# Optimization experiments

Measured on AMD Instinct MI355X. Metric: run time of the kernel, lower is better.

Reference implementation:

```python
import jax, jax.numpy as jnp
import numpy as np

NUM_EXPERTS = 64
TOP_K = 8
ALPHA = 0.001


def setup_inputs() -> dict:
    key = jax.random.key(0)
    k1, k2 = jax.random.split(key)
    hidden_states = jax.random.normal(k1, (16384, 2048), dtype=jnp.float32)
    # nn.Linear(D, E) weight has shape (E, D); init ~ N(0, 1/sqrt(D))
    weight = jax.random.normal(k2, (NUM_EXPERTS, 2048), dtype=jnp.float32) / jnp.sqrt(2048.0)
    return {"hidden_states": hidden_states, "weight": weight}


def reference(hidden_states, weight):
    # Router logits: (N, E)
    logits = jnp.einsum("nd,ed->ne", hidden_states, weight)
    scores = jax.nn.softmax(logits, axis=-1)

    # top-k (lax.top_k returns sorted values; torch used sorted=False, same set)
    topk_weights, topk_indices = jax.lax.top_k(scores, TOP_K)  # (N, K)
    topk_weights = topk_weights / jnp.sum(topk_weights, axis=-1, keepdims=True)

    # Aux load-balancing loss (training path). Instead of materializing a
    # (N, K, E) one-hot tensor, count tokens per expert with a scatter-add.
    num_tokens = hidden_states.shape[0]
    counts = jnp.zeros((NUM_EXPERTS,), dtype=jnp.float32).at[topk_indices.ravel()].add(1.0)
    tokens_per_expert = counts / (num_tokens * TOP_K)
    mean_prob = jnp.mean(scores, axis=0)  # (E,)
    aux_loss = ALPHA * NUM_EXPERTS * jnp.sum(tokens_per_expert * mean_prob)

    return topk_weights, topk_indices, aux_loss
```

## Files before the change

kernel.cpp:

```cpp
#include <hip/hip_runtime.h>
#include <hip/hip_bf16.h>

#define N_TOKENS 16384
#define DIM      2048
#define NEXP     64
#define TOPK     8
#define LOSCALE  2048.0f
#define NBLOCKS  512
#define TOKPB    32
#define LSTRIDE  66
#define NREP     32
#define NROUNDS  16
#define NBUF     3
#define BUFSZ    (TOKPB * 128)

typedef _Float16 half8   __attribute__((ext_vector_type(8)));
typedef float    floatx4 __attribute__((ext_vector_type(4)));

__global__ __launch_bounds__(256) void wprep_kernel(const float* __restrict__ W,
                                                    _Float16* __restrict__ Whi,
                                                    _Float16* __restrict__ Wlo) {
    int i = blockIdx.x * 256 + threadIdx.x;
    float w = W[i];
    _Float16 h = (_Float16)w;
    Whi[i] = h;
    Wlo[i] = (_Float16)((w - (float)h) * LOSCALE);
}

__device__ __forceinline__ void gl_lds16(const float* src, float* lds_base, int byteoff) {
    __builtin_amdgcn_global_load_lds(
        (const __attribute__((address_space(1))) unsigned int*)src,
        (__attribute__((address_space(3))) unsigned int*)((char*)lds_base + byteoff),
        16, 0, 0);
}

__device__ __forceinline__ void split8(const floatx4& f0, const floatx4& f1,
                                       half8& H, half8& L) {
    #pragma unroll
    for (int j = 0; j < 4; ++j) {
        _Float16 h = (_Float16)f0[j];
        H[j] = h; L[j] = (_Float16)((f0[j] - (float)h) * LOSCALE);
    }
    #pragma unroll
    for (int j = 0; j < 4; ++j) {
        _Float16 h = (_Float16)f1[j];
        H[4 + j] = h; L[4 + j] = (_Float16)((f1[j] - (float)h) * LOSCALE);
    }
}

__global__ __launch_bounds__(256) void moe_kernel(const float* __restrict__ A,
                                                  const _Float16* __restrict__ Whi,
                                                  const _Float16* __restrict__ Wlo,
                                                  float* __restrict__ out_w,
                                                  float* __restrict__ out_i,
                                                  float* __restrict__ out_aux,
                                                  float* __restrict__ cnt_ws,
                                                  float* __restrict__ sp_ws,
                                                  unsigned int* __restrict__ ticket) {
    __shared__ float stage[NBUF][BUFSZ];
    __shared__ float xch[TOKPB * LSTRIDE];
    __shared__ float s_cnt[NEXP];
    __shared__ float s_sp[NEXP];
    __shared__ int   s_last;

    const int tid   = threadIdx.x;
    const int lane  = tid & 63;
    const int wv    = tid >> 6;
    const int row16 = lane & 15;
    const int quad  = lane >> 4;
    const int tbase = blockIdx.x * TOKPB;

    if (tid < NEXP) { s_cnt[tid] = 0.f; s_sp[tid] = 0.f; }

    const float* asrc[4];
    #pragma unroll
    for (int j = 0; j < 4; ++j) {
        int tok  = (wv * 4 + j) * 2 + (lane >> 5);
        int colb = ((lane & 31) * 16) ^ ((tok & 7) << 4);
        asrc[j] = (const float*)((const char*)(A + (size_t)(tbase + tok) * DIM) + colb);
    }

    const _Float16* bhp = Whi + (size_t)(wv * 16 + row16) * DIM + quad * 8;
    const _Float16* blp = Wlo + (size_t)(wv * 16 + row16) * DIM + quad * 8;

    floatx4 acc0[2] = {};
    floatx4 acc1[2] = {};

    const int c0 = (quad * 8) ^ ((row16 & 7) * 4);

    #pragma unroll
    for (int j = 0; j < 4; ++j) gl_lds16(asrc[j],       &stage[0][0], (wv * 4 + j) * 1024);
    #pragma unroll
    for (int j = 0; j < 4; ++j) gl_lds16(asrc[j] + 128, &stage[1][0], (wv * 4 + j) * 1024);

    half8 bh[4], bl[4];
    #pragma unroll
    for (int c = 0; c < 4; ++c) {
        bh[c] = *(const half8*)(bhp + c * 32);
        bl[c] = *(const half8*)(blp + c * 32);
    }
    asm volatile("s_waitcnt vmcnt(12)" ::: "memory");
    __builtin_amdgcn_sched_barrier(0);
    __builtin_amdgcn_s_barrier();
    __builtin_amdgcn_sched_barrier(0);

    #pragma unroll
    for (int r = 0; r < NROUNDS; ++r) {
        const float* rb = &stage[r % 3][0];

        if (r < NROUNDS - 2) {
            #pragma unroll
            for (int j = 0; j < 4; ++j)
                gl_lds16(asrc[j] + (r + 2) * 128, &stage[(r + 2) % 3][0], (wv * 4 + j) * 1024);
        }

        #pragma unroll
        for (int I = 0; I < 4; ++I) {
            const float* p0 = rb + row16 * 128 + I * 32;
            floatx4 f0 = *(const floatx4*)(p0 + c0);
            floatx4 f1 = *(const floatx4*)(p0 + (c0 ^ 4));
            half8 ah, al; split8(f0, f1, ah, al);
            acc0[0] = __builtin_amdgcn_mfma_f32_16x16x32_f16(ah, bh[I], acc0[0], 0, 0, 0);
            acc1[0] = __builtin_amdgcn_mfma_f32_16x16x32_f16(ah, bl[I], acc1[0], 0, 0, 0);
            acc1[0] = __builtin_amdgcn_mfma_f32_16x16x32_f16(al, bh[I], acc1[0], 0, 0, 0);

            const float* p1 = rb + (16 + row16) * 128 + I * 32;
            f0 = *(const floatx4*)(p1 + c0);
            f1 = *(const floatx4*)(p1 + (c0 ^ 4));
            split8(f0, f1, ah, al);
            acc0[1] = __builtin_amdgcn_mfma_f32_16x16x32_f16(ah, bh[I], acc0[1], 0, 0, 0);
            acc1[1] = __builtin_amdgcn_mfma_f32_16x16x32_f16(ah, bl[I], acc1[1], 0, 0, 0);
            acc1[1] = __builtin_amdgcn_mfma_f32_16x16x32_f16(al, bh[I], acc1[1], 0, 0, 0);

            if (r < NROUNDS - 1) {
                bh[I] = *(const half8*)(bhp + ((r + 1) * 4 + I) * 32);
                bl[I] = *(const half8*)(blp + ((r + 1) * 4 + I) * 32);
            }
        }

        if (r < NROUNDS - 2) {
            asm volatile("s_waitcnt vmcnt(12)" ::: "memory");
        } else if (r == NROUNDS - 2) {
            asm volatile("s_waitcnt vmcnt(8)" ::: "memory");
        }
        if (r < NROUNDS - 1) {
            __builtin_amdgcn_sched_barrier(0);
            __builtin_amdgcn_s_barrier();
            __builtin_amdgcn_sched_barrier(0);
        }
    }

    const float inv = 1.0f / LOSCALE;
    #pragma unroll
    for (int mt = 0; mt < 2; ++mt)
        #pragma unroll
        for (int reg = 0; reg < 4; ++reg) {
            int tok = mt * 16 + quad * 4 + reg;
            xch[tok * LSTRIDE + wv * 16 + row16] = acc0[mt][reg] + acc1[mt][reg] * inv;
        }
    __syncthreads();

    float sp = 0.f, cnt = 0.f;
    for (int i = 0; i < 8; ++i) {
        int t = wv * 8 + i;
        float lg = xch[t * LSTRIDE + lane];

        float m = lg;
        #pragma unroll
        for (int off = 32; off; off >>= 1) m = fmaxf(m, __shfl_xor(m, off));
        float e = expf(lg - m);
        float ssum = e;
        #pragma unroll
        for (int off = 32; off; off >>= 1) ssum += __shfl_xor(ssum, off);
        float score = e / ssum;
        sp += score;

        int rank = 0;
        #pragma unroll
        for (int j = 0; j < 64; ++j) {
            float sj = __shfl(score, j);
            rank += (sj > score) || (sj == score && j < lane);
        }
        bool sel = rank < TOPK;

        float v = sel ? score : 0.f;
        #pragma unroll
        for (int off = 32; off; off >>= 1) v += __shfl_xor(v, off);

        if (sel) {
            out_w[(size_t)(tbase + t) * TOPK + rank] = score / v;
            out_i[(size_t)(tbase + t) * TOPK + rank] = (float)lane;
            cnt += 1.f;
        }
    }

    atomicAdd(&s_sp[lane], sp);
    atomicAdd(&s_cnt[lane], cnt);
    __syncthreads();
    const int rep = (blockIdx.x & (NREP - 1)) * NEXP;
    if (tid < 64)       atomicAdd(&cnt_ws[rep + tid], s_cnt[tid]);
    else if (tid < 128) atomicAdd(&sp_ws[rep + tid - 64], s_sp[tid - 64]);

    __threadfence();
    __syncthreads();
    if (tid == 0)
        s_last = (atomicAdd(ticket, 1u) == (unsigned)(gridDim.x - 1));
    __syncthreads();
    if (s_last && tid < 64) {
        float c = 0.f, p = 0.f;
        #pragma unroll
        for (int rr = 0; rr < NREP; ++rr) {
            c += atomicAdd(&cnt_ws[rr * NEXP + tid], 0.f);
            p += atomicAdd(&sp_ws [rr * NEXP + tid], 0.f);
        }
        float v = (c / (float)(N_TOKENS * TOPK)) * (p / (float)N_TOKENS);
        #pragma unroll
        for (int off = 32; off; off >>= 1) v += __shfl_xor(v, off);
        if (tid == 0) out_aux[0] = 0.001f * (float)NEXP * v;
    }
}

extern "C" void kernel_launch(void* const* d_in, const int* in_sizes, int n_in,
                              void* d_out, int out_size, void* d_ws, size_t ws_size,
                              hipStream_t stream) {
    const float* A = (const float*)d_in[0];
    const float* W = (const float*)d_in[1];
    float* out = (float*)d_out;

    _Float16*     whi    = (_Float16*)d_ws;
    _Float16*     wlo    = whi + (size_t)NEXP * DIM;
    float*        cnt_ws = (float*)(wlo + (size_t)NEXP * DIM);
    float*        sp_ws  = cnt_ws + (size_t)NREP * NEXP;
    unsigned int* ticket = (unsigned int*)(sp_ws + (size_t)NREP * NEXP);

    hipMemsetAsync(cnt_ws, 0, 2 * NREP * NEXP * sizeof(float) + sizeof(unsigned int), stream);

    hipLaunchKernelGGL(wprep_kernel, dim3(NEXP * DIM / 256), dim3(256), 0, stream,
                       W, whi, wlo);

    float* out_w = out;
    float* out_i = out + (size_t)N_TOKENS * TOPK;
    float* out_a = out + 2 * (size_t)N_TOKENS * TOPK;

    hipLaunchKernelGGL(moe_kernel, dim3(NBLOCKS), dim3(256), 0, stream,
                       A, whi, wlo, out_w, out_i, out_a, cnt_ws, sp_ws, ticket);
}
```

Before: 256.6 us.

## Restructure A staging into double-buffered 256-wide K rounds with padded LDS rows

Measured after the change: 253.0 us. About the same (-1.4%).

```diff
diff --git a/kernel.cpp b/kernel.cpp
--- a/kernel.cpp
+++ b/kernel.cpp
@@ -10,9 +10,9 @@
 #define TOKPB    32
 #define LSTRIDE  66
 #define NREP     32
-#define NROUNDS  16
-#define NBUF     3
-#define BUFSZ    (TOKPB * 128)
+#define KROUND   256
+#define NR       8
+#define SPAD     260
 
 typedef _Float16 half8   __attribute__((ext_vector_type(8)));
 typedef float    floatx4 __attribute__((ext_vector_type(4)));
@@ -27,10 +27,10 @@
     Wlo[i] = (_Float16)((w - (float)h) * LOSCALE);
 }
 
-__device__ __forceinline__ void gl_lds16(const float* src, float* lds_base, int byteoff) {
+__device__ __forceinline__ void gl_lds16(const float* src, float* lds_dst) {
     __builtin_amdgcn_global_load_lds(
         (const __attribute__((address_space(1))) unsigned int*)src,
-        (__attribute__((address_space(3))) unsigned int*)((char*)lds_base + byteoff),
+        (__attribute__((address_space(3))) unsigned int*)lds_dst,
         16, 0, 0);
 }
 
@@ -57,7 +57,7 @@
                                                   float* __restrict__ cnt_ws,
                                                   float* __restrict__ sp_ws,
                                                   unsigned int* __restrict__ ticket) {
-    __shared__ float stage[NBUF][BUFSZ];
+    __shared__ float stage[2][TOKPB][SPAD];
     __shared__ float xch[TOKPB * LSTRIDE];
     __shared__ float s_cnt[NEXP];
     __shared__ float s_sp[NEXP];
@@ -72,81 +72,67 @@
 
     if (tid < NEXP) { s_cnt[tid] = 0.f; s_sp[tid] = 0.f; }
 
-    const float* asrc[4];
-    #pragma unroll
-    for (int j = 0; j < 4; ++j) {
-        int tok  = (wv * 4 + j) * 2 + (lane >> 5);
-        int colb = ((lane & 31) * 16) ^ ((tok & 7) << 4);
-        asrc[j] = (const float*)((const char*)(A + (size_t)(tbase + tok) * DIM) + colb);
-    }
+    const float* asrc[8];
+    #pragma unroll
+    for (int i = 0; i < 8; ++i)
+        asrc[i] = A + (size_t)(tbase + wv * 8 + i) * DIM + lane * 4;
 
     const _Float16* bhp = Whi + (size_t)(wv * 16 + row16) * DIM + quad * 8;
     const _Float16* blp = Wlo + (size_t)(wv * 16 + row16) * DIM + quad * 8;
 
     floatx4 acc0[2] = {};
     floatx4 acc1[2] = {};
-
-    const int c0 = (quad * 8) ^ ((row16 & 7) * 4);
-
-    #pragma unroll
-    for (int j = 0; j < 4; ++j) gl_lds16(asrc[j],       &stage[0][0], (wv * 4 + j) * 1024);
-    #pragma unroll
-    for (int j = 0; j < 4; ++j) gl_lds16(asrc[j] + 128, &stage[1][0], (wv * 4 + j) * 1024);
-
-    half8 bh[4], bl[4];
-    #pragma unroll
-    for (int c = 0; c < 4; ++c) {
+    half8 bh[8], bl[8];
+
+    #pragma unroll
+    for (int i = 0; i < 8; ++i) gl_lds16(asrc[i], &stage[0][wv * 8 + i][0]);
+    #pragma unroll
+    for (int c = 0; c < 8; ++c) {
         bh[c] = *(const half8*)(bhp + c * 32);
         bl[c] = *(const half8*)(blp + c * 32);
     }
-    asm volatile("s_waitcnt vmcnt(12)" ::: "memory");
+    #pragma unroll
+    for (int i = 0; i < 8; ++i) gl_lds16(asrc[i] + KROUND, &stage[1][wv * 8 + i][0]);
+
+    __builtin_amdgcn_sched_barrier(0);
+    asm volatile("s_waitcnt vmcnt(8)" ::: "memory");
     __builtin_amdgcn_sched_barrier(0);
     __builtin_amdgcn_s_barrier();
     __builtin_amdgcn_sched_barrier(0);
 
-    #pragma unroll
-    for (int r = 0; r < NROUNDS; ++r) {
-        const float* rb = &stage[r % 3][0];
-
-        if (r < NROUNDS - 2) {
+    for (int r = 0; r < NR; ++r) {
+        const float* sb = &stage[r & 1][0][0];
+
+        #pragma unroll
+        for (int c = 0; c < 8; ++c) {
             #pragma unroll
-            for (int j = 0; j < 4; ++j)
-                gl_lds16(asrc[j] + (r + 2) * 128, &stage[(r + 2) % 3][0], (wv * 4 + j) * 1024);
-        }
-
-        #pragma unroll
-        for (int I = 0; I < 4; ++I) {
-            const float* p0 = rb + row16 * 128 + I * 32;
-            floatx4 f0 = *(const floatx4*)(p0 + c0);
-            floatx4 f1 = *(const floatx4*)(p0 + (c0 ^ 4));
-            half8 ah, al; split8(f0, f1, ah, al);
-            acc0[0] = __builtin_amdgcn_mfma_f32_16x16x32_f16(ah, bh[I], acc0[0], 0, 0, 0);
-            acc1[0] = __builtin_amdgcn_mfma_f32_16x16x32_f16(ah, bl[I], acc1[0], 0, 0, 0);
-            acc1[0] = __builtin_amdgcn_mfma_f32_16x16x32_f16(al, bh[I], acc1[0], 0, 0, 0);
-
-            const float* p1 = rb + (16 + row16) * 128 + I * 32;
-            f0 = *(const floatx4*)(p1 + c0);
-            f1 = *(const floatx4*)(p1 + (c0 ^ 4));
-            split8(f0, f1, ah, al);
-            acc0[1] = __builtin_amdgcn_mfma_f32_16x16x32_f16(ah, bh[I], acc0[1], 0, 0, 0);
-            acc1[1] = __builtin_amdgcn_mfma_f32_16x16x32_f16(ah, bl[I], acc1[1], 0, 0, 0);
-            acc1[1] = __builtin_amdgcn_mfma_f32_16x16x32_f16(al, bh[I], acc1[1], 0, 0, 0);
-
-            if (r < NROUNDS - 1) {
-                bh[I] = *(const half8*)(bhp + ((r + 1) * 4 + I) * 32);
-                bl[I] = *(const half8*)(blp + ((r + 1) * 4 + I) * 32);
+            for (int mt = 0; mt < 2; ++mt) {
+                const float* p = sb + (mt * 16 + row16) * SPAD + c * 32 + quad * 8;
+                floatx4 f0 = *(const floatx4*)p;
+                floatx4 f1 = *(const floatx4*)(p + 4);
+                half8 ah, al; split8(f0, f1, ah, al);
+                acc0[mt] = __builtin_amdgcn_mfma_f32_16x16x32_f16(ah, bh[c], acc0[mt], 0, 0, 0);
+                acc1[mt] = __builtin_amdgcn_mfma_f32_16x16x32_f16(ah, bl[c], acc1[mt], 0, 0, 0);
+                acc1[mt] = __builtin_amdgcn_mfma_f32_16x16x32_f16(al, bh[c], acc1[mt], 0, 0, 0);
             }
         }
 
-        if (r < NROUNDS - 2) {
-            asm volatile("s_waitcnt vmcnt(12)" ::: "memory");
-        } else if (r == NROUNDS - 2) {
-            asm volatile("s_waitcnt vmcnt(8)" ::: "memory");
-        }
-        if (r < NROUNDS - 1) {
+        if (r < NR - 1) {
+            #pragma unroll
+            for (int c = 0; c < 8; ++c) {
+                bh[c] = *(const half8*)(bhp + (r + 1) * KROUND + c * 32);
+                bl[c] = *(const half8*)(blp + (r + 1) * KROUND + c * 32);
+            }
+            __builtin_amdgcn_sched_barrier(0);
+            asm volatile("s_waitcnt vmcnt(16)" ::: "memory");
             __builtin_amdgcn_sched_barrier(0);
             __builtin_amdgcn_s_barrier();
             __builtin_amdgcn_sched_barrier(0);
+            if (r < NR - 2) {
+                #pragma unroll
+                for (int i = 0; i < 8; ++i)
+                    gl_lds16(asrc[i] + (r + 2) * KROUND, &stage[r & 1][wv * 8 + i][0]);
+            }
         }
     }
 
```
